# Kernel optimization log

Hardware: AMD Instinct MI355X
Metric: run time of the kernel (lower is better)

The kernel has to match this reference:

```python
import jax, jax.numpy as jnp
import numpy as np

N_NODES = 50000
N_EDGES = 800000
N_GRAPHS = 512
VOCAB = 128
HID = 64
NCLS = 5


def _seg_mean(vals, ids, num_segments):
    s = jax.ops.segment_sum(vals, ids, num_segments=num_segments)
    cnt = jax.ops.segment_sum(jnp.ones((vals.shape[0],), vals.dtype), ids, num_segments=num_segments)
    return s / jnp.maximum(cnt, 1.0)[:, None]


def sage_conv(x, src, dst, W_l, b_l, W_r):
    # PyG SAGEConv (mean aggr): out = lin_l(mean_{j in N(i)} x_j) + lin_r(x_i)
    agg = _seg_mean(x[src], dst, x.shape[0])          # [N, H] gather + scatter-mean
    return agg @ W_l.T + b_l + x @ W_r.T


def setup_inputs() -> dict:
    key = jax.random.key(0)
    ks = jax.random.split(key, 10)
    scale = 1.0 / np.sqrt(HID)
    x_tokens = jax.random.randint(ks[0], (N_NODES,), 0, VOCAB)
    edge_index = jax.random.randint(ks[1], (2, N_EDGES), 0, N_NODES)
    batch = jnp.sort(jax.random.randint(ks[2], (N_NODES,), 0, N_GRAPHS))
    return {
        "x_tokens": x_tokens,
        "edge_index": edge_index,
        "batch": batch,
        "embed": jax.random.normal(ks[3], (VOCAB, HID), jnp.float32),
        "W1l": jax.random.normal(ks[4], (HID, HID), jnp.float32) * scale,
        "b1l": jnp.zeros((HID,), jnp.float32),
        "W1r": jax.random.normal(ks[5], (HID, HID), jnp.float32) * scale,
        "W2l": jax.random.normal(ks[6], (HID, HID), jnp.float32) * scale,
        "b2l": jnp.zeros((HID,), jnp.float32),
        "W2r": jax.random.normal(ks[7], (HID, HID), jnp.float32) * scale,
        "Wlin": jax.random.normal(ks[8], (NCLS, HID), jnp.float32) * scale,
        "blin": jnp.zeros((NCLS,), jnp.float32),
    }


def reference(x_tokens, edge_index, batch, embed, W1l, b1l, W1r, W2l, b2l, W2r, Wlin, blin):
    src, dst = edge_index[0], edge_index[1]
    x = embed[x_tokens]                                  # [N, H] embedding lookup
    x = jax.nn.relu(sage_conv(x, src, dst, W1l, b1l, W1r))
    x = jax.nn.relu(sage_conv(x, src, dst, W2l, b2l, W2r))
    g = _seg_mean(x, batch, N_GRAPHS)                    # global_mean_pool -> [G, H]
    return g @ Wlin.T + blin                             # [G, num_classes]
```

## Files before the change

kernel.cpp:

```cpp
#include <hip/hip_runtime.h>

#define N_NODES  50000
#define N_EDGES  800000
#define N_GRAPHS 512
#define HID      64
#define NCLS     5
#define NB       64
#define EST      36
#define AST      68

typedef __attribute__((ext_vector_type(8))) short bf16x8;
typedef __attribute__((ext_vector_type(4))) float f32x4;

__device__ inline unsigned short f2bf(float f) {
    unsigned int u = __builtin_bit_cast(unsigned int, f);
    unsigned int r = (u + 0x7FFFu + ((u >> 16) & 1u)) >> 16;
    return (unsigned short)r;
}
__device__ inline unsigned int packbf(float a, float b) {
    return (unsigned int)f2bf(a) | ((unsigned int)f2bf(b) << 16);
}
__device__ inline float bf2f(unsigned int u16) {
    unsigned int t = u16 << 16;
    return __builtin_bit_cast(float, t);
}

#define XCDS   8
#define NPX    (N_NODES / XCDS)
#define ECHUNK ((N_EDGES + 255) / 256)
#define SEC_E  (ECHUNK * XCDS * 256)
#define EBUF_T (128 * 32)
#define PW_T   (64 * 64)
#define PREP_T (SEC_E + EBUF_T + N_NODES + 2 * PW_T)
__global__ void k_prep_fill(
    const int* __restrict__ src, const int* __restrict__ dst,
    const int* __restrict__ tok,
    int* __restrict__ cnt, unsigned int* __restrict__ bucket,
    const float* __restrict__ embed, unsigned int* __restrict__ ebufg,
    const int* __restrict__ batch,
    int* __restrict__ pos_start, int* __restrict__ pos_end,
    const float* __restrict__ W1l, const float* __restrict__ W1r,
    unsigned int* __restrict__ wb1,
    const float* __restrict__ W2l, const float* __restrict__ W2r,
    unsigned int* __restrict__ wb2) {
    int gid = blockIdx.x * blockDim.x + threadIdx.x;
    if (gid < SEC_E) {
        int blk   = gid >> 8;
        int range = blk & 7;
        int e     = (blk >> 3) * 256 + (gid & 255);
        if (e < N_EDGES) {
            int d = dst[e];
            int s = src[e];
            int lo = range * NPX;
            if (d >= lo && d < lo + NPX) {
                unsigned int t = (unsigned int)tok[s];
                int pos = atomicAdd(&cnt[d], 1);
                if (pos < NB) bucket[(long)d * NB + pos] = (unsigned int)s | (t << 16);
            }
        }
        return;
    }
    gid -= SEC_E;
    if (gid < EBUF_T) {
        int t = gid >> 5, c = gid & 31;
        float2 v = ((const float2*)(embed + (long)t * HID))[c];
        ebufg[gid] = packbf(v.x, v.y);
        return;
    }
    gid -= EBUF_T;
    if (gid < N_NODES) {
        int n = gid;
        int b = batch[n];
        if (n == 0 || batch[n - 1] != b) pos_start[b] = n;
        if (n == N_NODES - 1 || batch[n + 1] != b) pos_end[b] = n + 1;
        return;
    }
    gid -= N_NODES;
    if (gid < 2 * PW_T) {
        const float* Wl = (gid < PW_T) ? W1l : W2l;
        const float* Wr = (gid < PW_T) ? W1r : W2r;
        unsigned int* wb = (gid < PW_T) ? wb1 : wb2;
        int i = (gid < PW_T) ? gid : gid - PW_T;
        int h = i >> 6, c = i & 63;
        float2 v = (c < 32) ? ((const float2*)(Wl + (long)h * HID))[c]
                            : ((const float2*)(Wr + (long)h * HID))[c - 32];
        wb[i] = packbf(v.x, v.y);
    }
}

template <bool L1>
__global__ __launch_bounds__(1024) void k_layer(
    const int* __restrict__ cnt, const unsigned int* __restrict__ bucket,
    const int* __restrict__ tok, const unsigned int* __restrict__ ebufg,
    const unsigned int* __restrict__ xb,
    const unsigned int* __restrict__ wb, const float* __restrict__ bl,
    unsigned short* __restrict__ xoutb)
{
    __shared__ unsigned int As[64 * AST];
    __shared__ unsigned int elds[L1 ? 128 * EST : 1];
    const int tid  = threadIdx.x;
    const int wv   = tid >> 6;
    const int lane = tid & 63;
    const int n0   = blockIdx.x * 64;

    if (L1) {
        for (int i = tid; i < EBUF_T; i += 1024) {
            int t = i >> 5, c = i & 31;
            elds[t * EST + c] = ebufg[i];
        }
        __syncthreads();
    }

    const int q  = lane & 7;
    const int e8 = lane >> 3;

#pragma unroll
    for (int i = 0; i < 4; ++i) {
        int rl = wv * 4 + i;
        int nn = n0 + rl;
        int nc = min(nn, N_NODES - 1);
        int deg = cnt[nc];
        int m   = (nn < N_NODES) ? min(deg, NB) : 0;
        unsigned int v = (lane < m) ? bucket[(long)nc * NB + lane] : 0u;
        float f0 = 0, f1 = 0, f2 = 0, f3 = 0, f4 = 0, f5 = 0, f6 = 0, f7 = 0;
#pragma unroll
        for (int g = 0; g < 8; ++g) {
            int j = g * 8 + e8;
            unsigned int vv = __shfl(v, j, 64);
            if (j < m) {
                uint4 w4;
                if (L1) w4 = *(const uint4*)(elds + (vv >> 16) * EST + q * 4);
                else    w4 = *((const uint4*)(xb + (long)(vv & 0xffffu) * 32) + q);
                f0 += bf2f(w4.x & 0xffff); f1 += bf2f(w4.x >> 16);
                f2 += bf2f(w4.y & 0xffff); f3 += bf2f(w4.y >> 16);
                f4 += bf2f(w4.z & 0xffff); f5 += bf2f(w4.z >> 16);
                f6 += bf2f(w4.w & 0xffff); f7 += bf2f(w4.w >> 16);
            }
        }
#pragma unroll
        for (int o = 8; o < 64; o <<= 1) {
            f0 += __shfl_xor(f0, o, 64); f1 += __shfl_xor(f1, o, 64);
            f2 += __shfl_xor(f2, o, 64); f3 += __shfl_xor(f3, o, 64);
            f4 += __shfl_xor(f4, o, 64); f5 += __shfl_xor(f5, o, 64);
            f6 += __shfl_xor(f6, o, 64); f7 += __shfl_xor(f7, o, 64);
        }
        if (e8 == 0) {
            float inv = 1.0f / (float)max(deg, 1);
            uint4 o;
            o.x = packbf(f0 * inv, f1 * inv);
            o.y = packbf(f2 * inv, f3 * inv);
            o.z = packbf(f4 * inv, f5 * inv);
            o.w = packbf(f6 * inv, f7 * inv);
            *(uint4*)(As + rl * AST + q * 4) = o;
        } else if (e8 == 1) {
            uint4 sv;
            if (L1) { int tk = tok[nc]; sv = *(const uint4*)(elds + tk * EST + q * 4); }
            else    { sv = *((const uint4*)(xb + (long)nc * 32) + q); }
            *(uint4*)(As + rl * AST + 32 + q * 4) = sv;
        }
    }
    __syncthreads();

    const int s    = wv & 3;
    const int t    = wv >> 2;
    const int mm   = lane & 15;
    const int quad = lane >> 4;

    bf16x8 afr[4];
#pragma unroll
    for (int kst = 0; kst < 4; ++kst)
        afr[kst] = *(const bf16x8*)(As + (s * 16 + mm) * AST + kst * 16 + quad * 4);

    f32x4 acc = (f32x4){0.f, 0.f, 0.f, 0.f};
#pragma unroll
    for (int kst = 0; kst < 4; ++kst) {
        bf16x8 bfr = *(const bf16x8*)(wb + (t * 16 + mm) * 64 + kst * 16 + quad * 4);
        acc = __builtin_amdgcn_mfma_f32_16x16x32_bf16(bfr, afr[kst], acc, 0, 0, 0);
    }

    int node = n0 + s * 16 + mm;
    if (node < N_NODES) {
        int hb = t * 16 + quad * 4;
        float4 bb = *(const float4*)(bl + hb);
        ushort4 o;
        o.x = f2bf(fmaxf(acc[0] + bb.x, 0.f));
        o.y = f2bf(fmaxf(acc[1] + bb.y, 0.f));
        o.z = f2bf(fmaxf(acc[2] + bb.z, 0.f));
        o.w = f2bf(fmaxf(acc[3] + bb.w, 0.f));
        *(ushort4*)(xoutb + (long)node * HID + hb) = o;
    }
}

__global__ __launch_bounds__(256) void k_pool(
    const unsigned int* __restrict__ x2b,
    const int* __restrict__ pos_start, const int* __restrict__ pos_end,
    const float* __restrict__ Wlin, const float* __restrict__ blin,
    float* __restrict__ out)
{
    __shared__ float part[4][8][8];
    int g    = blockIdx.x;
    int tid  = threadIdx.x;
    int wv   = tid >> 6;
    int lane = tid & 63;
    int q    = lane & 7;
    int slot = wv * 8 + (lane >> 3);
    int s = pos_start[g], e = pos_end[g];
    float f0 = 0, f1 = 0, f2 = 0, f3 = 0, f4 = 0, f5 = 0, f6 = 0, f7 = 0;
    for (int n = s + slot; n < e; n += 32) {
        uint4 v = *((const uint4*)(x2b + (long)n * 32) + q);
        f0 += bf2f(v.x & 0xffff); f1 += bf2f(v.x >> 16);
        f2 += bf2f(v.y & 0xffff); f3 += bf2f(v.y >> 16);
        f4 += bf2f(v.z & 0xffff); f5 += bf2f(v.z >> 16);
        f6 += bf2f(v.w & 0xffff); f7 += bf2f(v.w >> 16);
    }
#pragma unroll
    for (int o = 8; o < 64; o <<= 1) {
        f0 += __shfl_xor(f0, o, 64); f1 += __shfl_xor(f1, o, 64);
        f2 += __shfl_xor(f2, o, 64); f3 += __shfl_xor(f3, o, 64);
        f4 += __shfl_xor(f4, o, 64); f5 += __shfl_xor(f5, o, 64);
        f6 += __shfl_xor(f6, o, 64); f7 += __shfl_xor(f7, o, 64);
    }
    if (lane < 8) {
        part[wv][lane][0] = f0; part[wv][lane][1] = f1;
        part[wv][lane][2] = f2; part[wv][lane][3] = f3;
        part[wv][lane][4] = f4; part[wv][lane][5] = f5;
        part[wv][lane][6] = f6; part[wv][lane][7] = f7;
    }
    __syncthreads();
    if (wv == 0) {
        f0 = part[0][q][0] + part[1][q][0] + part[2][q][0] + part[3][q][0];
        f1 = part[0][q][1] + part[1][q][1] + part[2][q][1] + part[3][q][1];
        f2 = part[0][q][2] + part[1][q][2] + part[2][q][2] + part[3][q][2];
        f3 = part[0][q][3] + part[1][q][3] + part[2][q][3] + part[3][q][3];
        f4 = part[0][q][4] + part[1][q][4] + part[2][q][4] + part[3][q][4];
        f5 = part[0][q][5] + part[1][q][5] + part[2][q][5] + part[3][q][5];
        f6 = part[0][q][6] + part[1][q][6] + part[2][q][6] + part[3][q][6];
        f7 = part[0][q][7] + part[1][q][7] + part[2][q][7] + part[3][q][7];
        float inv = 1.0f / (float)max(e - s, 1);
        f0 *= inv; f1 *= inv; f2 *= inv; f3 *= inv;
        f4 *= inv; f5 *= inv; f6 *= inv; f7 *= inv;
#pragma unroll
        for (int c = 0; c < NCLS; ++c) {
            const float* wr = Wlin + c * HID + q * 8;
            float p = f0 * wr[0] + f1 * wr[1] + f2 * wr[2] + f3 * wr[3] +
                      f4 * wr[4] + f5 * wr[5] + f6 * wr[6] + f7 * wr[7];
            p += __shfl_xor(p, 1, 64);
            p += __shfl_xor(p, 2, 64);
            p += __shfl_xor(p, 4, 64);
            if (lane == 0) out[g * NCLS + c] = p + blin[c];
        }
    }
}

extern "C" void kernel_launch(void* const* d_in, const int* in_sizes, int n_in,
                              void* d_out, int out_size, void* d_ws, size_t ws_size,
                              hipStream_t stream) {
    const int*   tok   = (const int*)d_in[0];
    const int*   eidx  = (const int*)d_in[1];
    const int*   batch = (const int*)d_in[2];
    const float* embed = (const float*)d_in[3];
    const float* W1l   = (const float*)d_in[4];
    const float* b1l   = (const float*)d_in[5];
    const float* W1r   = (const float*)d_in[6];
    const float* W2l   = (const float*)d_in[7];
    const float* b2l   = (const float*)d_in[8];
    const float* W2r   = (const float*)d_in[9];
    const float* Wlin  = (const float*)d_in[10];
    const float* blin  = (const float*)d_in[11];
    float* out = (float*)d_out;

    const int* src = eidx;
    const int* dst = eidx + N_EDGES;

    char* wsp = (char*)d_ws;
    size_t off = 0;
    auto alloc = [&](size_t bytes) -> void* {
        void* p = wsp + off;
        off = (off + bytes + 255) & ~(size_t)255;
        return p;
    };
    int*   cnt     = (int*)  alloc((size_t)N_NODES * 4);
    int*   pstart  = (int*)  alloc((size_t)N_GRAPHS * 4);
    int*   pend    = (int*)  alloc((size_t)N_GRAPHS * 4);
    unsigned int* bucket = (unsigned int*)alloc((size_t)N_NODES * NB * 4);
    unsigned int* x1b    = (unsigned int*)alloc((size_t)N_NODES * 32 * 4);
    unsigned int* x2b    = (unsigned int*)alloc((size_t)N_NODES * 32 * 4);
    unsigned int* ebufg  = (unsigned int*)alloc((size_t)128 * 32 * 4);
    unsigned int* wb1    = (unsigned int*)alloc((size_t)64 * 64 * 4);
    unsigned int* wb2    = (unsigned int*)alloc((size_t)64 * 64 * 4);

    hipMemsetAsync(cnt, 0, (char*)pend - (char*)cnt + (size_t)N_GRAPHS * 4, stream);

    k_prep_fill<<<(PREP_T + 255) / 256, 256, 0, stream>>>(
        src, dst, tok, cnt, bucket,
        embed, ebufg, batch, pstart, pend, W1l, W1r, wb1, W2l, W2r, wb2);

    const int LBLK = (N_NODES + 63) / 64;
    k_layer<true><<<LBLK, 1024, 0, stream>>>(cnt, bucket, tok, ebufg, nullptr,
                                             wb1, b1l, (unsigned short*)x1b);
    k_layer<false><<<LBLK, 1024, 0, stream>>>(cnt, bucket, nullptr, nullptr, x1b,
                                              wb2, b2l, (unsigned short*)x2b);

    k_pool<<<N_GRAPHS, 256, 0, stream>>>(x2b, pstart, pend, Wlin, blin, out);
}
```

Baseline: 203.5 us.

## Assign edge-fill node ranges by hardware XCD id to localize atomics

Splits the edge bucket-fill out of the prep kernel into its own kernel. Each block reads its XCD id from a hardware register and claims that node range for its edge chunk through an atomic bitmask, falling back to a free range when taken. The goal is for each XCD to do its atomics and bucket writes on nodes owned by that XCD, keeping them in its local L2. The cost is an extra kernel launch, a per-chunk mask atomic with a spin loop, and a larger memset.

```diff
diff --git a/kernel.cpp b/kernel.cpp
--- a/kernel.cpp
+++ b/kernel.cpp
@@ -27,15 +27,43 @@
 
 #define XCDS   8
 #define NPX    (N_NODES / XCDS)
-#define ECHUNK ((N_EDGES + 255) / 256)
-#define SEC_E  (ECHUNK * XCDS * 256)
-#define EBUF_T (128 * 32)
-#define PW_T   (64 * 64)
-#define PREP_T (SEC_E + EBUF_T + N_NODES + 2 * PW_T)
-__global__ void k_prep_fill(
+#define CHUNKS (N_EDGES / 256)
+__global__ __launch_bounds__(256) void k_fill(
     const int* __restrict__ src, const int* __restrict__ dst,
     const int* __restrict__ tok,
     int* __restrict__ cnt, unsigned int* __restrict__ bucket,
+    unsigned int* __restrict__ mask)
+{
+    __shared__ int s_r;
+    int chunk = blockIdx.x % CHUNKS;
+    if (threadIdx.x == 0) {
+        unsigned int xcd;
+        asm volatile("s_getreg_b32 %0, hwreg(HW_REG_XCC_ID)" : "=s"(xcd));
+        int r = (int)(xcd & 7u);
+        unsigned int old = atomicOr(&mask[chunk], 1u << r);
+        while (old & (1u << r)) {
+            unsigned int freeb = (~old) & 0xFFu;
+            r = __ffs(freeb) - 1;
+            old = atomicOr(&mask[chunk], 1u << r);
+        }
+        s_r = r;
+    }
+    __syncthreads();
+    int r = s_r;
+    int e = chunk * 256 + threadIdx.x;
+    int d = dst[e];
+    int lo = r * NPX;
+    if (d < lo || d >= lo + NPX) return;
+    int s = src[e];
+    unsigned int t = (unsigned int)tok[s];
+    int pos = atomicAdd(&cnt[d], 1);
+    if (pos < NB) bucket[(long)d * NB + pos] = (unsigned int)s | (t << 16);
+}
+
+#define EBUF_T (128 * 32)
+#define PW_T   (64 * 64)
+#define PREP_T (EBUF_T + N_NODES + 2 * PW_T)
+__global__ void k_prep(
     const float* __restrict__ embed, unsigned int* __restrict__ ebufg,
     const int* __restrict__ batch,
     int* __restrict__ pos_start, int* __restrict__ pos_end,
@@ -44,23 +72,6 @@
     const float* __restrict__ W2l, const float* __restrict__ W2r,
     unsigned int* __restrict__ wb2) {
     int gid = blockIdx.x * blockDim.x + threadIdx.x;
-    if (gid < SEC_E) {
-        int blk   = gid >> 8;
-        int range = blk & 7;
-        int e     = (blk >> 3) * 256 + (gid & 255);
-        if (e < N_EDGES) {
-            int d = dst[e];
-            int s = src[e];
-            int lo = range * NPX;
-            if (d >= lo && d < lo + NPX) {
-                unsigned int t = (unsigned int)tok[s];
-                int pos = atomicAdd(&cnt[d], 1);
-                if (pos < NB) bucket[(long)d * NB + pos] = (unsigned int)s | (t << 16);
-            }
-        }
-        return;
-    }
-    gid -= SEC_E;
     if (gid < EBUF_T) {
         int t = gid >> 5, c = gid & 31;
         float2 v = ((const float2*)(embed + (long)t * HID))[c];
@@ -282,6 +293,7 @@
     int*   cnt     = (int*)  alloc((size_t)N_NODES * 4);
     int*   pstart  = (int*)  alloc((size_t)N_GRAPHS * 4);
     int*   pend    = (int*)  alloc((size_t)N_GRAPHS * 4);
+    unsigned int* mask = (unsigned int*)alloc((size_t)CHUNKS * 4);
     unsigned int* bucket = (unsigned int*)alloc((size_t)N_NODES * NB * 4);
     unsigned int* x1b    = (unsigned int*)alloc((size_t)N_NODES * 32 * 4);
     unsigned int* x2b    = (unsigned int*)alloc((size_t)N_NODES * 32 * 4);
@@ -289,10 +301,11 @@
     unsigned int* wb1    = (unsigned int*)alloc((size_t)64 * 64 * 4);
     unsigned int* wb2    = (unsigned int*)alloc((size_t)64 * 64 * 4);
 
-    hipMemsetAsync(cnt, 0, (char*)pend - (char*)cnt + (size_t)N_GRAPHS * 4, stream);
-
-    k_prep_fill<<<(PREP_T + 255) / 256, 256, 0, stream>>>(
-        src, dst, tok, cnt, bucket,
+    hipMemsetAsync(cnt, 0, (char*)(mask + CHUNKS) - (char*)cnt, stream);
+
+    k_fill<<<CHUNKS * XCDS, 256, 0, stream>>>(src, dst, tok, cnt, bucket, mask);
+
+    k_prep<<<(PREP_T + 255) / 256, 256, 0, stream>>>(
         embed, ebufg, batch, pstart, pend, W1l, W1r, wb1, W2l, W2r, wb2);
 
     const int LBLK = (N_NODES + 63) / 64;
```

After: 209.3 us. +2.9%, slower.
